# Performance work log

Measured on AMD Instinct MI355X. Metric: run time of the kernel, lower is better.

The kernel has to match this reference:

```python
import jax, jax.numpy as jnp
import numpy as np

B, OBS, ACT_DIM, C, CTX, H = 128, 512, 7, 100, 128, 512
IN = OBS + 1 + CTX  # states + scalar action component + context = 641


def cont2disc(values, n):
    return jnp.clip(jnp.floor((values + 1.0) / 2.0 * n), 0, n - 1)


def setup_inputs() -> dict:
    key = jax.random.key(0)
    ks = jax.random.split(key, 10)
    def w(k, shape):
        return jax.random.normal(k, shape, dtype=jnp.float32) / np.sqrt(shape[-2])
    return {
        "observations": jax.random.normal(ks[0], (B, OBS), dtype=jnp.float32),
        "actions": jax.random.uniform(ks[1], (B, ACT_DIM), dtype=jnp.float32, minval=-1.0, maxval=1.0),
        # one MLP per action dim (weight_sharing=False): layers IN->H->H->CTX
        "W1": w(ks[2], (ACT_DIM, IN, H)),  "b1": jnp.zeros((ACT_DIM, H), jnp.float32),
        "W2": w(ks[3], (ACT_DIM, H, H)),   "b2": jnp.zeros((ACT_DIM, H), jnp.float32),
        "W3": w(ks[4], (ACT_DIM, H, CTX)), "b3": jnp.zeros((ACT_DIM, CTX), jnp.float32),
        # output_proj = MLP((1,)): single dense CTX->1, no activation
        "Wp": w(ks[5], (CTX, 1)), "bp": jnp.zeros((1,), jnp.float32),
        "compute_lse": 1,
    }


def reference(observations, actions, W1, b1, W2, b2, W3, b3, Wp, bp, compute_lse):
    n = observations.shape[0]
    acts = cont2disc(actions, C)  # [B, ACT_DIM], float component indices
    context = jnp.zeros((n, CTX), observations.dtype)
    comp = jnp.arange(C, dtype=observations.dtype)  # candidate components 0..C-1
    q = jnp.zeros((n, ACT_DIM * C), observations.dtype)

    for i in range(1, ACT_DIM):
        def mlp(x, i=i):  # hidden layers relu, final layer linear
            h = jax.nn.relu(x @ W1[i] + b1[i])
            h = jax.nn.relu(h @ W2[i] + b2[i])
            return h @ W3[i] + b3[i]

        # batched over all num_components candidate actions (replaces the per-j loop)
        xin = jnp.concatenate([
            jnp.broadcast_to(observations[:, None, :], (n, C, OBS)),
            jnp.broadcast_to(comp[None, :, None], (n, C, 1)),
            jnp.broadcast_to(context[:, None, :], (n, C, CTX)),
        ], axis=-1)  # [B, C, IN]
        curr_ctx = mlp(xin) + context[:, None, :]        # [B, C, CTX]
        qv = (curr_ctx @ Wp + bp)[..., 0]                # [B, C]
        q = q.at[:, (i - 1) * C : i * C].set(qv)          # which_qval ordering

        # advance context with the actual (discretized) action
        x = jnp.concatenate([observations, acts[:, i:i + 1], context], axis=-1)
        context = mlp(x) + context

    if compute_lse:
        return jax.scipy.special.logsumexp(q, axis=-1)    # [B]
    return context @ Wp + bp                              # [B, 1]
```

## Files before the change

kernel.cpp:

```cpp
#include <hip/hip_runtime.h>
#include <math.h>

#define BATCH 128
#define ACT 7
#define NC 100
#define CTXD 128
#define HID 512
#define QW 600

typedef __attribute__((ext_vector_type(8))) __bf16 bf16x8;
typedef __attribute__((ext_vector_type(4))) float f32x4;
typedef __attribute__((ext_vector_type(4))) unsigned short u16x4;

__device__ __forceinline__ unsigned short f2bf(float f) {
    union { float f; unsigned int u; } v; v.f = f;
    unsigned int u = v.u;
    return (unsigned short)((u + 0x7fffu + ((u >> 16) & 1u)) >> 16);
}
__device__ __forceinline__ unsigned int pack2bf(float a, float b) {
    unsigned int ua = __float_as_uint(a) + 0x8000u;
    unsigned int ub = __float_as_uint(b) + 0x8000u;
    return (ua >> 16) | (ub & 0xffff0000u);
}

__device__ __forceinline__ void async16(const void* g, void* l) {
    __builtin_amdgcn_global_load_lds(
        (const __attribute__((address_space(1))) unsigned int*)(uintptr_t)g,
        (__attribute__((address_space(3))) unsigned int*)(unsigned int)(uintptr_t)l,
        16, 0, 0);
}

__global__ void prep_kernel(const float* __restrict__ obs, const float* __restrict__ W1,
                            const float* __restrict__ W2, const float* __restrict__ W3,
                            const float* __restrict__ Wp,
                            unsigned short* __restrict__ obs_bf, unsigned short* __restrict__ W1Cbf,
                            unsigned short* __restrict__ W2bf, unsigned short* __restrict__ W3bf,
                            unsigned short* __restrict__ W1AT, unsigned short* __restrict__ W2T,
                            float* __restrict__ vq) {
    const int bidx = blockIdx.x, tid = threadIdx.x;
    if (bidx < 2368) {
        const int e = (bidx * 256 + tid) * 4;
        const float* src; unsigned short* dst;
        if (e < 65536)        { src = obs + e; dst = obs_bf + e; }
        else if (e < 458752)  { int f = e - 65536; int i = f >> 16; int rem = f & 65535;
                                src = W1 + (size_t)(i + 1) * 328192 + 513*512 + rem; dst = W1Cbf + f; }
        else if (e < 2031616) { int f = e - 458752; src = W2 + 262144 + f; dst = W2bf + f; }
        else                  { int f = e - 2031616; src = W3 + 65536 + f; dst = W3bf + f; }
        float4 v = *(const float4*)src;
        u16x4 o; o[0] = f2bf(v.x); o[1] = f2bf(v.y); o[2] = f2bf(v.z); o[3] = f2bf(v.w);
        *(u16x4*)dst = o;
    } else if (bidx < 5440) {
        __shared__ float tile[32][33];
        const int idx = bidx - 2368;
        const int z = idx >> 8, rem = idx & 255;
        const int rb = rem & 15, cb = rem >> 4;
        const float* ip; unsigned short* op;
        if (z < 6) { ip = W1 + (size_t)(z + 1) * 328192; op = W1AT + (size_t)z * 262144; }
        else       { int i = z - 6; ip = W2 + (size_t)(i + 1) * 262144; op = W2T + (size_t)i * 262144; }
        const int r0 = rb * 32, c0 = cb * 32;
        const int tx = tid & 31, ty = tid >> 5;
        #pragma unroll
        for (int j = 0; j < 32; j += 8)
            tile[ty + j][tx] = ip[(size_t)(r0 + ty + j) * 512 + c0 + tx];
        __syncthreads();
        #pragma unroll
        for (int j = 0; j < 32; j += 8)
            op[(size_t)(c0 + ty + j) * 512 + r0 + tx] = f2bf(tile[tx][ty + j]);
    } else {
        const int idx = bidx - 5440;
        const int z = idx >> 1, k = (idx & 1) * 256 + tid;
        const float4* row = (const float4*)(W3 + (size_t)(z + 1) * 65536 + (size_t)k * 128);
        const float4* wp4 = (const float4*)Wp;
        float s = 0.f;
        #pragma unroll 8
        for (int n = 0; n < 32; ++n) {
            float4 a = row[n], w = wp4[n];
            s += a.x*w.x + a.y*w.y + a.z*w.z + a.w*w.w;
        }
        vq[z * 512 + k] = s;
    }
}

__launch_bounds__(256)
__global__ void yobs_kernel(const unsigned short* __restrict__ A,
                            const unsigned short* __restrict__ BtAll,
                            const float* __restrict__ b1,
                            float* __restrict__ Yobs) {
    __shared__ unsigned short As[64*32];
    __shared__ unsigned short Bs[128*32];
    const int m0 = blockIdx.x * 64;
    const int n0 = blockIdx.y * 128;
    const int z  = blockIdx.z;
    const unsigned short* Bt = BtAll + (size_t)z * 262144;
    const int tid = threadIdx.x, lane = tid & 63, wave = tid >> 6;
    const int wm = wave >> 1, wn = wave & 1;
    const int srow = tid >> 2, skc = (tid & 3) * 8;
    const unsigned short* gA  = A  + (size_t)(m0 + srow) * HID + skc;
    const unsigned short* gB0 = Bt + (size_t)(n0 + srow) * HID + skc;
    const unsigned short* gB1 = gB0 + 64 * HID;
    f32x4 acc[2][4] = {};
    for (int k0 = 0; k0 < HID; k0 += 32) {
        async16(gA + k0, As + tid*8);
        async16(gB0 + k0, Bs + tid*8);
        async16(gB1 + k0, Bs + 2048 + tid*8);
        __syncthreads();
        const int q8 = (lane >> 4) * 8, l15 = lane & 15;
        bf16x8 af[2], bfr[4];
        #pragma unroll
        for (int mt = 0; mt < 2; ++mt)
            af[mt] = *(const bf16x8*)(As + (wm*32 + mt*16 + l15) * 32 + q8);
        #pragma unroll
        for (int nt = 0; nt < 4; ++nt)
            bfr[nt] = *(const bf16x8*)(Bs + (wn*64 + nt*16 + l15) * 32 + q8);
        #pragma unroll
        for (int mt = 0; mt < 2; ++mt)
            #pragma unroll
            for (int nt = 0; nt < 4; ++nt)
                acc[mt][nt] = __builtin_amdgcn_mfma_f32_16x16x32_bf16(af[mt], bfr[nt], acc[mt][nt], 0, 0, 0);
        __syncthreads();
    }
    const int colL = wn*64 + (lane & 15);
    #pragma unroll
    for (int nt = 0; nt < 4; ++nt) {
        const int col = n0 + colL + nt*16;
        const float bb = b1[(z + 1) * HID + col];
        #pragma unroll
        for (int mt = 0; mt < 2; ++mt)
            #pragma unroll
            for (int r = 0; r < 4; ++r) {
                const int row = m0 + wm*32 + mt*16 + (lane >> 4)*4 + r;
                Yobs[(size_t)z * 65536 + (size_t)row * HID + col] = acc[mt][nt][r] + bb;
            }
    }
}

__launch_bounds__(1024)
__global__ void chain_kernel(const float* __restrict__ Yobs, const float* __restrict__ W1,
                             const unsigned short* __restrict__ W1Cbf,
                             const unsigned short* __restrict__ W2bf,
                             const unsigned short* __restrict__ W3bf,
                             const float* __restrict__ b2, const float* __restrict__ b3,
                             const float* __restrict__ actions,
                             const float* __restrict__ Wp, const float* __restrict__ bp,
                             float* __restrict__ Y0all, float* __restrict__ QOFF) {
    const int b = blockIdx.x, t = threadIdx.x;
    __shared__ float ctx[128], h1[512], h2s[512];
    __shared__ float part[2048];
    const int pair = t & 255, kq = t >> 8;
    const int pair3 = t & 63, kq3 = t >> 6;
    if (t < 128) ctx[t] = 0.f;
    __syncthreads();
    for (int i = 1; i <= 6; ++i) {
        if (t < 128) part[t] = (ctx[t] + b3[i*128 + t]) * Wp[t];
        __syncthreads();
        if (t < 64) {
            float v = part[t] + part[t + 64];
            #pragma unroll
            for (int o = 32; o > 0; o >>= 1) v += __shfl_down(v, o, 64);
            if (t == 0) QOFF[(i-1)*128 + b] = v + bp[0];
        }
        __syncthreads();
        const float a = actions[b*ACT + i];
        float fj = floorf((a + 1.0f) * 50.0f);
        fj = fminf(fmaxf(fj, 0.0f), 99.0f);
        {
            const unsigned int* wp1 = (const unsigned int*)(W1Cbf + (size_t)(i-1)*65536) + pair;
            float acc0 = 0.f, acc1 = 0.f;
            #pragma unroll 8
            for (int k = kq*32; k < kq*32 + 32; ++k) {
                unsigned int u = wp1[k*256];
                float c = ctx[k];
                acc0 = fmaf(c, __uint_as_float(u << 16), acc0);
                acc1 = fmaf(c, __uint_as_float(u & 0xffff0000u), acc1);
            }
            *(float2*)(&part[kq*512 + 2*pair]) = make_float2(acc0, acc1);
        }
        __syncthreads();
        if (t < 256) {
            const int n2 = 2*t;
            float2 p0 = *(const float2*)(&part[n2]);
            float2 p1 = *(const float2*)(&part[512 + n2]);
            float2 p2 = *(const float2*)(&part[1024 + n2]);
            float2 p3 = *(const float2*)(&part[1536 + n2]);
            float2 yo = *(const float2*)(Yobs + (size_t)(i-1)*65536 + b*512 + n2);
            float y0a = yo.x + p0.x + p1.x + p2.x + p3.x;
            float y0b = yo.y + p0.y + p1.y + p2.y + p3.y;
            *(float2*)(Y0all + (size_t)(i-1)*65536 + b*512 + n2) = make_float2(y0a, y0b);
            const float* w1a = W1 + (size_t)i*328192 + 262144;
            float2 wv = *(const float2*)(w1a + n2);
            h1[n2]   = fmaxf(fmaf(fj, wv.x, y0a), 0.f);
            h1[n2+1] = fmaxf(fmaf(fj, wv.y, y0b), 0.f);
        }
        __syncthreads();
        {
            const unsigned int* wp2 = (const unsigned int*)(W2bf + (size_t)(i-1)*262144) + pair;
            float acc0 = 0.f, acc1 = 0.f;
            #pragma unroll 16
            for (int k = kq*128; k < kq*128 + 128; ++k) {
                unsigned int u = wp2[k*256];
                float hv = h1[k];
                acc0 = fmaf(hv, __uint_as_float(u << 16), acc0);
                acc1 = fmaf(hv, __uint_as_float(u & 0xffff0000u), acc1);
            }
            *(float2*)(&part[kq*512 + 2*pair]) = make_float2(acc0, acc1);
        }
        __syncthreads();
        if (t < 256) {
            const int n2 = 2*t;
            float2 p0 = *(const float2*)(&part[n2]);
            float2 p1 = *(const float2*)(&part[512 + n2]);
            float2 p2 = *(const float2*)(&part[1024 + n2]);
            float2 p3 = *(const float2*)(&part[1536 + n2]);
            float2 bb = *(const float2*)(b2 + i*512 + n2);
            h2s[n2]   = fmaxf(p0.x + p1.x + p2.x + p3.x + bb.x, 0.f);
            h2s[n2+1] = fmaxf(p0.y + p1.y + p2.y + p3.y + bb.y, 0.f);
        }
        __syncthreads();
        {
            const unsigned int* wp3 = (const unsigned int*)(W3bf + (size_t)(i-1)*65536) + pair3;
            float acc0 = 0.f, acc1 = 0.f;
            #pragma unroll 8
            for (int k = kq3*32; k < kq3*32 + 32; ++k) {
                unsigned int u = wp3[k*64];
                float hv = h2s[k];
                acc0 = fmaf(hv, __uint_as_float(u << 16), acc0);
                acc1 = fmaf(hv, __uint_as_float(u & 0xffff0000u), acc1);
            }
            *(float2*)(&part[kq3*128 + 2*pair3]) = make_float2(acc0, acc1);
        }
        __syncthreads();
        if (t < 128) {
            float s = 0.f;
            #pragma unroll
            for (int qg = 0; qg < 16; ++qg) s += part[qg*128 + t];
            ctx[t] = s + b3[i*128 + t] + ctx[t];
        }
        __syncthreads();
    }
}

__global__ void h1all_kernel(const float* __restrict__ Y0all, const float* __restrict__ W1,
                             unsigned short* __restrict__ H1) {
    const int t = blockIdx.x * 256 + threadIdx.x;
    const int row = t >> 6, kc = (t & 63) << 3;
    const int z = row / 12800, rr = row - z * 12800;
    const int b = rr / 100;
    const float c = (float)(rr - b * 100);
    const float* yp = Y0all + (size_t)z*65536 + (size_t)b*512 + kc;
    const float* wp = W1 + (size_t)(z+1)*328192 + 262144 + kc;
    float4 ya = *(const float4*)(yp), yb = *(const float4*)(yp + 4);
    float4 wa = *(const float4*)(wp), wb = *(const float4*)(wp + 4);
    uint4 o;
    o.x = pack2bf(fmaxf(fmaf(c, wa.x, ya.x), 0.f), fmaxf(fmaf(c, wa.y, ya.y), 0.f));
    o.y = pack2bf(fmaxf(fmaf(c, wa.z, ya.z), 0.f), fmaxf(fmaf(c, wa.w, ya.w), 0.f));
    o.z = pack2bf(fmaxf(fmaf(c, wb.x, yb.x), 0.f), fmaxf(fmaf(c, wb.y, yb.y), 0.f));
    o.w = pack2bf(fmaxf(fmaf(c, wb.z, yb.z), 0.f), fmaxf(fmaf(c, wb.w, yb.w), 0.f));
    *(uint4*)(H1 + (size_t)row * 512 + kc) = o;
}

__launch_bounds__(256)
__global__ void gemm2q_kernel(const unsigned short* __restrict__ H1,
                              const unsigned short* __restrict__ W2T,
                              const float* __restrict__ b2,
                              const float* __restrict__ vq, float* __restrict__ qpart) {
    __shared__ unsigned short As[2][4096];
    __shared__ unsigned short Bs[2][4096];
    const int bidx = blockIdx.x;
    const int xcd = bidx & 7, seq = bidx >> 3;
    const int plane = seq & 3;
    const int rt = xcd * 75 + (seq >> 2);
    const int z  = rt / 100;
    const int r0 = rt * 128;
    const int n0 = plane * 128;
    const int tid = threadIdx.x, lane = tid & 63, wave = tid >> 6;
    const int wm = wave >> 1, wn = wave & 1;
    const int srow = tid >> 2, skc = (tid & 3) * 8;
    const int l15 = lane & 15, q8 = (lane >> 4) * 8;
    const unsigned short* gA0 = H1 + (size_t)(r0 + srow)*512 + skc;
    const unsigned short* gA1 = gA0 + 64*512;
    const unsigned short* gB0 = W2T + (size_t)z*262144 + (size_t)(n0 + srow)*512 + skc;
    const unsigned short* gB1 = gB0 + 64*512;
    f32x4 acc[4][4] = {};
    for (int k0 = 0; k0 < 512; k0 += 64) {
        async16(gA0 + k0,      &As[0][tid*8]);
        async16(gA1 + k0,      &As[0][2048 + tid*8]);
        async16(gA0 + k0 + 32, &As[1][tid*8]);
        async16(gA1 + k0 + 32, &As[1][2048 + tid*8]);
        async16(gB0 + k0,      &Bs[0][tid*8]);
        async16(gB1 + k0,      &Bs[0][2048 + tid*8]);
        async16(gB0 + k0 + 32, &Bs[1][tid*8]);
        async16(gB1 + k0 + 32, &Bs[1][2048 + tid*8]);
        __syncthreads();
        #pragma unroll
        for (int h = 0; h < 2; ++h) {
            bf16x8 af[4], bfr[4];
            #pragma unroll
            for (int mt = 0; mt < 4; ++mt)
                af[mt] = *(const bf16x8*)(&As[h][(wm*64 + mt*16 + l15)*32 + q8]);
            #pragma unroll
            for (int nt = 0; nt < 4; ++nt)
                bfr[nt] = *(const bf16x8*)(&Bs[h][(wn*64 + nt*16 + l15)*32 + q8]);
            #pragma unroll
            for (int mt = 0; mt < 4; ++mt)
                #pragma unroll
                for (int nt = 0; nt < 4; ++nt)
                    acc[mt][nt] = __builtin_amdgcn_mfma_f32_16x16x32_bf16(af[mt], bfr[nt], acc[mt][nt], 0, 0, 0);
        }
        __syncthreads();
    }
    float vb[4], bb[4];
    #pragma unroll
    for (int nt = 0; nt < 4; ++nt) {
        const int col = n0 + wn*64 + nt*16 + l15;
        bb[nt] = b2[(z+1)*512 + col];
        vb[nt] = vq[z*512 + col];
    }
    const int plane2 = plane * 2 + wn;
    const int gq = lane >> 4;
    #pragma unroll
    for (int mt = 0; mt < 4; ++mt)
        #pragma unroll
        for (int r = 0; r < 4; ++r) {
            float p = 0.f;
            #pragma unroll
            for (int nt = 0; nt < 4; ++nt)
                p = fmaf(fmaxf(acc[mt][nt][r] + bb[nt], 0.f), vb[nt], p);
            p += __shfl_xor(p, 1, 64);
            p += __shfl_xor(p, 2, 64);
            p += __shfl_xor(p, 4, 64);
            p += __shfl_xor(p, 8, 64);
            if (l15 == 0) {
                const int grow = r0 + wm*64 + mt*16 + gq*4 + r;
                qpart[(size_t)plane2 * 76800 + grow] = p;
            }
        }
}

__global__ void lse_kernel(const float* __restrict__ qpart, const float* __restrict__ QOFF,
                           float* __restrict__ out) {
    __shared__ float red[256];
    __shared__ float qs[QW];
    const int b = blockIdx.x, t = threadIdx.x;
    for (int k = t; k < QW; k += 256) {
        const int z = k / 100, gc = k - z * 100;
        const int grow = z * 12800 + b * 100 + gc;
        float s = QOFF[z * 128 + b];
        #pragma unroll
        for (int p = 0; p < 8; ++p) s += qpart[(size_t)p * 76800 + grow];
        qs[k] = s;
    }
    __syncthreads();
    float m = 0.0f;
    for (int k = t; k < QW; k += 256) m = fmaxf(m, qs[k]);
    red[t] = m; __syncthreads();
    for (int s = 128; s > 0; s >>= 1) { if (t < s) red[t] = fmaxf(red[t], red[t+s]); __syncthreads(); }
    m = red[0]; __syncthreads();
    float sum = 0.0f;
    for (int k = t; k < QW; k += 256) sum += expf(qs[k] - m);
    red[t] = sum; __syncthreads();
    for (int s = 128; s > 0; s >>= 1) { if (t < s) red[t] += red[t+s]; __syncthreads(); }
    if (t == 0) out[b] = logf(red[0] + 100.0f * expf(-m)) + m;
}

extern "C" void kernel_launch(void* const* d_in, const int* in_sizes, int n_in,
                              void* d_out, int out_size, void* d_ws, size_t ws_size,
                              hipStream_t stream) {
    const float* obs     = (const float*)d_in[0];
    const float* actions = (const float*)d_in[1];
    const float* W1      = (const float*)d_in[2];
    const float* b1      = (const float*)d_in[3];
    const float* W2      = (const float*)d_in[4];
    const float* b2      = (const float*)d_in[5];
    const float* W3      = (const float*)d_in[6];
    const float* b3      = (const float*)d_in[7];
    const float* Wp      = (const float*)d_in[8];
    const float* bp      = (const float*)d_in[9];
    float* out = (float*)d_out;
    float* ws  = (float*)d_ws;

    unsigned short* obs_bf = (unsigned short*)(ws);
    unsigned short* W1AT   = (unsigned short*)(ws + 32768);
    unsigned short* W2T    = (unsigned short*)(ws + 819200);
    unsigned short* W1Cbf  = (unsigned short*)(ws + 1605632);
    unsigned short* W2bf   = (unsigned short*)(ws + 1802240);
    unsigned short* W3bf   = (unsigned short*)(ws + 2588672);
    float* Yobs  = ws + 2785280;
    float* Y0all = ws + 3178496;
    float* QOFF  = ws + 3571712;
    float* vq    = ws + 3572736;
    float* qpart = ws + 3575808;
    unsigned short* H1 = (unsigned short*)(ws + 4190208);

    prep_kernel<<<5452, 256, 0, stream>>>(obs, W1, W2, W3, Wp,
                                          obs_bf, W1Cbf, W2bf, W3bf, W1AT, W2T, vq);
    yobs_kernel<<<dim3(2,4,6), 256, 0, stream>>>(obs_bf, W1AT, b1, Yobs);
    chain_kernel<<<BATCH, 1024, 0, stream>>>(Yobs, W1, W1Cbf, W2bf, W3bf, b2, b3, actions, Wp, bp, Y0all, QOFF);
    h1all_kernel<<<19200, 256, 0, stream>>>(Y0all, W1, H1);
    gemm2q_kernel<<<2400, 256, 0, stream>>>(H1, W2T, b2, vq, qpart);
    lse_kernel<<<BATCH, 256, 0, stream>>>(qpart, QOFF, out);
}
```

Measured before the change: 234.5 us.

## Replace candidate-sweep GEMM with piecewise-linear event sweep over ReLU breakpoints

Because the first-layer pre-activation is affine in the candidate index c, each hidden unit switches on or off at most once across the 100 candidates. The layer-2 pre-activation is therefore piecewise linear in c. The new sweep kernel finds each unit's breakpoint, sorts the events by candidate with a shared-memory counting sort, and keeps running A + c*B accumulators in fp32. This removes the H1 materialization, the bf16 W2 transpose and the large MFMA GEMM, along with the qpart partial buffers. The cost is serial per-block event processing with many wave shuffles and data-dependent breakpoint arithmetic that must exactly match the floor and ReLU boundaries.

```diff
diff --git a/kernel.cpp b/kernel.cpp
--- a/kernel.cpp
+++ b/kernel.cpp
@@ -17,11 +17,6 @@
     unsigned int u = v.u;
     return (unsigned short)((u + 0x7fffu + ((u >> 16) & 1u)) >> 16);
 }
-__device__ __forceinline__ unsigned int pack2bf(float a, float b) {
-    unsigned int ua = __float_as_uint(a) + 0x8000u;
-    unsigned int ub = __float_as_uint(b) + 0x8000u;
-    return (ua >> 16) | (ub & 0xffff0000u);
-}
 
 __device__ __forceinline__ void async16(const void* g, void* l) {
     __builtin_amdgcn_global_load_lds(
@@ -35,8 +30,7 @@
                             const float* __restrict__ Wp,
                             unsigned short* __restrict__ obs_bf, unsigned short* __restrict__ W1Cbf,
                             unsigned short* __restrict__ W2bf, unsigned short* __restrict__ W3bf,
-                            unsigned short* __restrict__ W1AT, unsigned short* __restrict__ W2T,
-                            float* __restrict__ vq) {
+                            unsigned short* __restrict__ W1AT, float* __restrict__ vq) {
     const int bidx = blockIdx.x, tid = threadIdx.x;
     if (bidx < 2368) {
         const int e = (bidx * 256 + tid) * 4;
@@ -49,14 +43,13 @@
         float4 v = *(const float4*)src;
         u16x4 o; o[0] = f2bf(v.x); o[1] = f2bf(v.y); o[2] = f2bf(v.z); o[3] = f2bf(v.w);
         *(u16x4*)dst = o;
-    } else if (bidx < 5440) {
+    } else if (bidx < 3904) {
         __shared__ float tile[32][33];
         const int idx = bidx - 2368;
         const int z = idx >> 8, rem = idx & 255;
         const int rb = rem & 15, cb = rem >> 4;
-        const float* ip; unsigned short* op;
-        if (z < 6) { ip = W1 + (size_t)(z + 1) * 328192; op = W1AT + (size_t)z * 262144; }
-        else       { int i = z - 6; ip = W2 + (size_t)(i + 1) * 262144; op = W2T + (size_t)i * 262144; }
+        const float* ip = W1 + (size_t)(z + 1) * 328192;
+        unsigned short* op = W1AT + (size_t)z * 262144;
         const int r0 = rb * 32, c0 = cb * 32;
         const int tx = tid & 31, ty = tid >> 5;
         #pragma unroll
@@ -67,7 +60,7 @@
         for (int j = 0; j < 32; j += 8)
             op[(size_t)(c0 + ty + j) * 512 + r0 + tx] = f2bf(tile[tx][ty + j]);
     } else {
-        const int idx = bidx - 5440;
+        const int idx = bidx - 3904;
         const int z = idx >> 1, k = (idx & 1) * 256 + tid;
         const float4* row = (const float4*)(W3 + (size_t)(z + 1) * 65536 + (size_t)k * 128);
         const float4* wp4 = (const float4*)Wp;
@@ -239,116 +232,146 @@
     }
 }
 
-__global__ void h1all_kernel(const float* __restrict__ Y0all, const float* __restrict__ W1,
-                             unsigned short* __restrict__ H1) {
-    const int t = blockIdx.x * 256 + threadIdx.x;
-    const int row = t >> 6, kc = (t & 63) << 3;
-    const int z = row / 12800, rr = row - z * 12800;
-    const int b = rr / 100;
-    const float c = (float)(rr - b * 100);
-    const float* yp = Y0all + (size_t)z*65536 + (size_t)b*512 + kc;
-    const float* wp = W1 + (size_t)(z+1)*328192 + 262144 + kc;
-    float4 ya = *(const float4*)(yp), yb = *(const float4*)(yp + 4);
-    float4 wa = *(const float4*)(wp), wb = *(const float4*)(wp + 4);
-    uint4 o;
-    o.x = pack2bf(fmaxf(fmaf(c, wa.x, ya.x), 0.f), fmaxf(fmaf(c, wa.y, ya.y), 0.f));
-    o.y = pack2bf(fmaxf(fmaf(c, wa.z, ya.z), 0.f), fmaxf(fmaf(c, wa.w, ya.w), 0.f));
-    o.z = pack2bf(fmaxf(fmaf(c, wb.x, yb.x), 0.f), fmaxf(fmaf(c, wb.y, yb.y), 0.f));
-    o.w = pack2bf(fmaxf(fmaf(c, wb.z, yb.z), 0.f), fmaxf(fmaf(c, wb.w, yb.w), 0.f));
-    *(uint4*)(H1 + (size_t)row * 512 + kc) = o;
-}
-
-__launch_bounds__(256)
-__global__ void gemm2q_kernel(const unsigned short* __restrict__ H1,
-                              const unsigned short* __restrict__ W2T,
-                              const float* __restrict__ b2,
-                              const float* __restrict__ vq, float* __restrict__ qpart) {
-    __shared__ unsigned short As[2][4096];
-    __shared__ unsigned short Bs[2][4096];
-    const int bidx = blockIdx.x;
-    const int xcd = bidx & 7, seq = bidx >> 3;
-    const int plane = seq & 3;
-    const int rt = xcd * 75 + (seq >> 2);
-    const int z  = rt / 100;
-    const int r0 = rt * 128;
-    const int n0 = plane * 128;
-    const int tid = threadIdx.x, lane = tid & 63, wave = tid >> 6;
-    const int wm = wave >> 1, wn = wave & 1;
-    const int srow = tid >> 2, skc = (tid & 3) * 8;
-    const int l15 = lane & 15, q8 = (lane >> 4) * 8;
-    const unsigned short* gA0 = H1 + (size_t)(r0 + srow)*512 + skc;
-    const unsigned short* gA1 = gA0 + 64*512;
-    const unsigned short* gB0 = W2T + (size_t)z*262144 + (size_t)(n0 + srow)*512 + skc;
-    const unsigned short* gB1 = gB0 + 64*512;
-    f32x4 acc[4][4] = {};
-    for (int k0 = 0; k0 < 512; k0 += 64) {
-        async16(gA0 + k0,      &As[0][tid*8]);
-        async16(gA1 + k0,      &As[0][2048 + tid*8]);
-        async16(gA0 + k0 + 32, &As[1][tid*8]);
-        async16(gA1 + k0 + 32, &As[1][2048 + tid*8]);
-        async16(gB0 + k0,      &Bs[0][tid*8]);
-        async16(gB1 + k0,      &Bs[0][2048 + tid*8]);
-        async16(gB0 + k0 + 32, &Bs[1][tid*8]);
-        async16(gB1 + k0 + 32, &Bs[1][2048 + tid*8]);
-        __syncthreads();
-        #pragma unroll
-        for (int h = 0; h < 2; ++h) {
-            bf16x8 af[4], bfr[4];
-            #pragma unroll
-            for (int mt = 0; mt < 4; ++mt)
-                af[mt] = *(const bf16x8*)(&As[h][(wm*64 + mt*16 + l15)*32 + q8]);
-            #pragma unroll
-            for (int nt = 0; nt < 4; ++nt)
-                bfr[nt] = *(const bf16x8*)(&Bs[h][(wn*64 + nt*16 + l15)*32 + q8]);
-            #pragma unroll
-            for (int mt = 0; mt < 4; ++mt)
-                #pragma unroll
-                for (int nt = 0; nt < 4; ++nt)
-                    acc[mt][nt] = __builtin_amdgcn_mfma_f32_16x16x32_bf16(af[mt], bfr[nt], acc[mt][nt], 0, 0, 0);
-        }
-        __syncthreads();
-    }
-    float vb[4], bb[4];
+__launch_bounds__(512)
+__global__ void sweep_kernel(const float* __restrict__ Y0all, const float* __restrict__ W1,
+                             const float* __restrict__ W2, const float* __restrict__ b2,
+                             const float* __restrict__ vq, const float* __restrict__ QOFF,
+                             float* __restrict__ q) {
+    __shared__ int cnt[101];
+    __shared__ int off[101];
+    __shared__ int off2[101];
+    __shared__ short ek[1040];
+    __shared__ short ebk[1040];
+    __shared__ float esy[1040], esw[1040];
+    __shared__ float wred[800];
+    const int bx = blockIdx.x;
+    const int z = bx >> 7, b = bx & 127;
+    const int t = threadIdx.x;
+    const float y = Y0all[(size_t)z*65536 + (size_t)b*512 + t];
+    const float w = W1[(size_t)(z+1)*328192 + 262144 + t];
+    if (t < 101) cnt[t] = 0;
+    __syncthreads();
+    const bool act0 = (y > 0.f);
+    int bk2 = -1; float s2 = 0.f;
+    if (act0 && w < 0.f) {
+        float r = -y / w;
+        if (r < 100.f) {
+            int c1 = (int)ceilf(r);
+            if (c1 > 1 && fmaf((float)(c1 - 1), w, y) <= 0.f) c1--;
+            if (fmaf((float)c1, w, y) > 0.f) c1++;
+            if (c1 >= 1 && c1 <= 99) { bk2 = c1; s2 = -1.f; }
+        }
+    } else if (!act0 && w > 0.f) {
+        float r = -y / w;
+        if (r < 100.f) {
+            int c0 = (int)floorf(r) + 1;
+            if (c0 > 1 && fmaf((float)(c0 - 1), w, y) > 0.f) c0--;
+            if (fmaf((float)c0, w, y) <= 0.f) c0++;
+            if (c0 >= 1 && c0 <= 99) { bk2 = c0; s2 = 1.f; }
+        }
+    }
+    if (act0) atomicAdd(&cnt[0], 1);
+    if (bk2 >= 0) atomicAdd(&cnt[bk2], 1);
+    __syncthreads();
+    if (t == 0) {
+        int acc = 0;
+        #pragma unroll 4
+        for (int c = 0; c < 101; ++c) { off[c] = acc; acc += cnt[c]; }
+    }
+    __syncthreads();
+    if (t < 101) off2[t] = off[t];
+    __syncthreads();
+    if (act0) {
+        int p = atomicAdd(&off2[0], 1);
+        ek[p] = (short)t; ebk[p] = 0; esy[p] = y; esw[p] = w;
+    }
+    if (bk2 >= 0) {
+        int p = atomicAdd(&off2[bk2], 1);
+        ek[p] = (short)t; ebk[p] = (short)bk2; esy[p] = s2 * y; esw[p] = s2 * w;
+    }
+    __syncthreads();
+    const int E0 = off[100];
+    const int Epad = (E0 + 7) & ~7;
+    if (t < 8 && E0 + t < Epad) {
+        ek[E0 + t] = 0; ebk[E0 + t] = 100; esy[E0 + t] = 0.f; esw[E0 + t] = 0.f;
+    }
+    __syncthreads();
+    const float b2n = b2[(z+1)*512 + t];
+    const float vn  = vq[z*512 + t];
+    const float* W2z = W2 + (size_t)(z+1)*262144 + t;
+    float A = 0.f, B = 0.f;
+    int cnext = 0;
+    const int lane = t & 63, wid = t >> 6;
+    float cwv[8], cdy[8], cdw[8]; int cbk[8];
     #pragma unroll
-    for (int nt = 0; nt < 4; ++nt) {
-        const int col = n0 + wn*64 + nt*16 + l15;
-        bb[nt] = b2[(z+1)*512 + col];
-        vb[nt] = vq[z*512 + col];
-    }
-    const int plane2 = plane * 2 + wn;
-    const int gq = lane >> 4;
-    #pragma unroll
-    for (int mt = 0; mt < 4; ++mt)
-        #pragma unroll
-        for (int r = 0; r < 4; ++r) {
-            float p = 0.f;
-            #pragma unroll
-            for (int nt = 0; nt < 4; ++nt)
-                p = fmaf(fmaxf(acc[mt][nt][r] + bb[nt], 0.f), vb[nt], p);
-            p += __shfl_xor(p, 1, 64);
-            p += __shfl_xor(p, 2, 64);
-            p += __shfl_xor(p, 4, 64);
-            p += __shfl_xor(p, 8, 64);
-            if (l15 == 0) {
-                const int grow = r0 + wm*64 + mt*16 + gq*4 + r;
-                qpart[(size_t)plane2 * 76800 + grow] = p;
-            }
-        }
-}
-
-__global__ void lse_kernel(const float* __restrict__ qpart, const float* __restrict__ QOFF,
-                           float* __restrict__ out) {
+    for (int j = 0; j < 8; ++j) {
+        if (j < Epad) {
+            int k = ek[j]; cbk[j] = ebk[j]; cdy[j] = esy[j]; cdw[j] = esw[j];
+            cwv[j] = W2z[(size_t)k * 512];
+        } else { cbk[j] = 100; cdy[j] = 0.f; cdw[j] = 0.f; cwv[j] = 0.f; }
+    }
+    for (int e0 = 0; e0 < Epad; e0 += 8) {
+        float nwv[8], ndy[8], ndw[8]; int nbk[8];
+        const int n0e = e0 + 8;
+        if (n0e < Epad) {
+            #pragma unroll
+            for (int j = 0; j < 8; ++j) {
+                int k = ek[n0e + j]; nbk[j] = ebk[n0e + j];
+                ndy[j] = esy[n0e + j]; ndw[j] = esw[n0e + j];
+                nwv[j] = W2z[(size_t)k * 512];
+            }
+        }
+        #pragma unroll
+        for (int j = 0; j < 8; ++j) {
+            while (cnext < cbk[j]) {
+                float h = fmaf((float)cnext, B, A) + b2n;
+                float en = fmaxf(h, 0.f) * vn;
+                en += __shfl_xor(en, 32, 64);
+                en += __shfl_xor(en, 16, 64);
+                en += __shfl_xor(en, 8, 64);
+                en += __shfl_xor(en, 4, 64);
+                en += __shfl_xor(en, 2, 64);
+                en += __shfl_xor(en, 1, 64);
+                if (lane == 0) wred[cnext * 8 + wid] = en;
+                ++cnext;
+                if (cnext > 99) break;
+            }
+            A = fmaf(cdy[j], cwv[j], A);
+            B = fmaf(cdw[j], cwv[j], B);
+        }
+        if (n0e < Epad) {
+            #pragma unroll
+            for (int j = 0; j < 8; ++j) {
+                cwv[j] = nwv[j]; cdy[j] = ndy[j]; cdw[j] = ndw[j]; cbk[j] = nbk[j];
+            }
+        }
+    }
+    while (cnext <= 99) {
+        float h = fmaf((float)cnext, B, A) + b2n;
+        float en = fmaxf(h, 0.f) * vn;
+        en += __shfl_xor(en, 32, 64);
+        en += __shfl_xor(en, 16, 64);
+        en += __shfl_xor(en, 8, 64);
+        en += __shfl_xor(en, 4, 64);
+        en += __shfl_xor(en, 2, 64);
+        en += __shfl_xor(en, 1, 64);
+        if (lane == 0) wred[cnext * 8 + wid] = en;
+        ++cnext;
+    }
+    __syncthreads();
+    if (t < 100) {
+        float s = 0.f;
+        #pragma unroll
+        for (int p = 0; p < 8; ++p) s += wred[t * 8 + p];
+        q[b * QW + z * 100 + t] = s + QOFF[z * 128 + b];
+    }
+}
+
+__global__ void lse_kernel(const float* __restrict__ q, float* __restrict__ out) {
     __shared__ float red[256];
     __shared__ float qs[QW];
     const int b = blockIdx.x, t = threadIdx.x;
-    for (int k = t; k < QW; k += 256) {
-        const int z = k / 100, gc = k - z * 100;
-        const int grow = z * 12800 + b * 100 + gc;
-        float s = QOFF[z * 128 + b];
-        #pragma unroll
-        for (int p = 0; p < 8; ++p) s += qpart[(size_t)p * 76800 + grow];
-        qs[k] = s;
-    }
+    for (int k = t; k < QW; k += 256) qs[k] = q[b * QW + k];
     __syncthreads();
     float m = 0.0f;
     for (int k = t; k < QW; k += 256) m = fmaxf(m, qs[k]);
@@ -380,22 +403,19 @@
 
     unsigned short* obs_bf = (unsigned short*)(ws);
     unsigned short* W1AT   = (unsigned short*)(ws + 32768);
-    unsigned short* W2T    = (unsigned short*)(ws + 819200);
-    unsigned short* W1Cbf  = (unsigned short*)(ws + 1605632);
-    unsigned short* W2bf   = (unsigned short*)(ws + 1802240);
-    unsigned short* W3bf   = (unsigned short*)(ws + 2588672);
-    float* Yobs  = ws + 2785280;
-    float* Y0all = ws + 3178496;
-    float* QOFF  = ws + 3571712;
-    float* vq    = ws + 3572736;
-    float* qpart = ws + 3575808;
-    unsigned short* H1 = (unsigned short*)(ws + 4190208);
-
-    prep_kernel<<<5452, 256, 0, stream>>>(obs, W1, W2, W3, Wp,
-                                          obs_bf, W1Cbf, W2bf, W3bf, W1AT, W2T, vq);
+    unsigned short* W1Cbf  = (unsigned short*)(ws + 819200);
+    unsigned short* W2bf   = (unsigned short*)(ws + 1015808);
+    unsigned short* W3bf   = (unsigned short*)(ws + 1802240);
+    float* Yobs  = ws + 1998848;
+    float* Y0all = ws + 2392064;
+    float* QOFF  = ws + 2785280;
+    float* vq    = ws + 2786304;
+    float* q     = ws + 2789376;
+
+    prep_kernel<<<3916, 256, 0, stream>>>(obs, W1, W2, W3, Wp,
+                                          obs_bf, W1Cbf, W2bf, W3bf, W1AT, vq);
     yobs_kernel<<<dim3(2,4,6), 256, 0, stream>>>(obs_bf, W1AT, b1, Yobs);
     chain_kernel<<<BATCH, 1024, 0, stream>>>(Yobs, W1, W1Cbf, W2bf, W3bf, b2, b3, actions, Wp, bp, Y0all, QOFF);
-    h1all_kernel<<<19200, 256, 0, stream>>>(Y0all, W1, H1);
-    gemm2q_kernel<<<2400, 256, 0, stream>>>(H1, W2T, b2, vq, qpart);
-    lse_kernel<<<BATCH, 256, 0, stream>>>(qpart, QOFF, out);
-}
+    sweep_kernel<<<768, 512, 0, stream>>>(Y0all, W1, W2, b2, vq, QOFF, q);
+    lse_kernel<<<BATCH, 256, 0, stream>>>(q, out);
+}
```

Result: slower. 321.8 us (+37.3%).
